# Kernel tuning notes

Measured on AMD Instinct MI355X. Metric: run time of the kernel, lower is better.

Reference implementation:

```python
import jax, jax.numpy as jnp
import numpy as np

B, T, A, F, K, DQ, DV = 64, 1024, 128, 1024, 31, 1024, 512  # filters F == T required by source math


def setup_inputs() -> dict:
    key = jax.random.key(0)
    ks = jax.random.split(key, 8)
    s = 0.05
    return {
        "query": jax.random.normal(ks[0], (B, 1, DQ), jnp.float32),
        "value": jax.random.normal(ks[1], (B, T, DV), jnp.float32),
        "attention_weights_cat": jax.random.uniform(ks[2], (B, T, 2), jnp.float32),
        "Wq": jax.random.normal(ks[3], (DQ, A), jnp.float32) * s,
        "Wm": jax.random.normal(ks[4], (DV, A), jnp.float32) * s,
        "Wv": jax.random.normal(ks[5], (A, 1), jnp.float32) * s,
        "Wconv": jax.random.normal(ks[6], (K, 2, F), jnp.float32) * s,
        "Wloc": jax.random.normal(ks[7], (T, A), jnp.float32) * s,
    }


def reference(query, value, attention_weights_cat, Wq, Wm, Wv, Wconv, Wloc):
    # query_layer: Dense(tanh, no bias): [B,1,DQ] -> [B,1,A]
    q = jnp.tanh(jnp.einsum('bld,da->bla', query, Wq))
    # memory_layer: Dense(tanh, no bias): [B,T,DV] -> [B,T,A]
    v = jnp.tanh(jnp.einsum('btd,da->bta', value, Wm))
    # location conv (SAME, no bias): [B,T,2] -> [B,T,F]
    loc = jax.lax.conv_general_dilated(
        attention_weights_cat, Wconv, window_strides=(1,), padding='SAME',
        dimension_numbers=('NWC', 'WIO', 'NWC'))
    # source transposes [0,2,1] then Dense(T->A, tanh): [B,F,T] -> [B,F,A]
    loc = jnp.tanh(jnp.einsum('bft,ta->bfa', jnp.transpose(loc, (0, 2, 1)), Wloc))
    # additive score (F == T so broadcast add is element-aligned): [B,T,1]
    score = jnp.einsum('bta,ao->bto', jnp.tanh(q + v + loc), Wv)
    alignment = jax.nn.softmax(score, axis=1)                # softmax over time
    context = jnp.sum(alignment * v, axis=1)                  # [B,A]
    return context, jnp.transpose(alignment, (0, 2, 1))       # [B,1,T]
```

## Files before the change

kernel.cpp:

```cpp
#include <hip/hip_runtime.h>
#include <hip/hip_bf16.h>

#define BB 64
#define TT 1024
#define AA 128
#define FF 1024
#define DQ 1024
#define DV 512

typedef __bf16 bf16x8_t __attribute__((ext_vector_type(8)));
typedef __bf16 bf16x4_t __attribute__((ext_vector_type(4)));
typedef float f32x4_t __attribute__((ext_vector_type(4)));
typedef _Float16 f16x4_t __attribute__((ext_vector_type(4)));

__device__ __forceinline__ float ftanh(float x) {
    float e = __expf(2.0f * x);
    return 1.0f - 2.0f / (e + 1.0f);
}

__device__ __forceinline__ __bf16 bhi(float x) { return (__bf16)x; }
__device__ __forceinline__ __bf16 blo(float x) {
    __bf16 h = (__bf16)x;
    return (__bf16)(x - (float)h);
}

__global__ __launch_bounds__(256) void k_prep(
    const float* __restrict__ Wm, const float* __restrict__ Wconv,
    const float* __restrict__ Wloc, const float* __restrict__ query,
    const float* __restrict__ Wq,
    __bf16* __restrict__ pwmhi, __bf16* __restrict__ pwmlo,
    __bf16* __restrict__ wcthi, __bf16* __restrict__ wctlo,
    __bf16* __restrict__ pwlhi, __bf16* __restrict__ pwllo,
    float* __restrict__ q_ws) {
    __shared__ float ls[128 * 65];
    int bx = blockIdx.x, tid = threadIdx.x;
    if (bx < 16) {
        int s = bx, d0 = s * 32;
        for (int i = tid; i < 4096; i += 256) {
            int dd = i >> 7, a = i & 127;
            ls[a * 33 + dd] = Wm[(d0 + dd) * AA + a];
        }
        __syncthreads();
#pragma unroll
        for (int u = 0; u < 2; u++) {
            int pos = tid * 2 + u;
            int l15 = pos & 15, lq = (pos >> 4) & 3, g = pos >> 6;
            bf16x8_t h8, l8;
#pragma unroll
            for (int j = 0; j < 8; j++) {
                float x = ls[(g * 16 + l15) * 33 + lq * 8 + j];
                h8[j] = bhi(x);
                l8[j] = blo(x);
            }
            size_t off = (size_t)(s * 512 + pos) * 8;
            *(bf16x8_t*)(pwmhi + off) = h8;
            *(bf16x8_t*)(pwmlo + off) = l8;
        }
    } else if (bx < 24) {
        int f0 = (bx - 16) * 128;
        for (int i = tid; i < 8192; i += 256) {
            int kc = i >> 7, f = i & 127;
            ls[f * 65 + kc] = (kc < 62) ? Wconv[kc * FF + f0 + f] : 0.f;
        }
        __syncthreads();
        int f = tid >> 1, half = tid & 1;
#pragma unroll
        for (int g = 0; g < 4; g++) {
            bf16x8_t h8, l8;
#pragma unroll
            for (int j = 0; j < 8; j++) {
                float x = ls[f * 65 + half * 32 + g * 8 + j];
                h8[j] = bhi(x);
                l8[j] = blo(x);
            }
            size_t off = (size_t)(f0 + f) * 64 + half * 32 + g * 8;
            *(bf16x8_t*)(wcthi + off) = h8;
            *(bf16x8_t*)(wctlo + off) = l8;
        }
    } else if (bx < 56) {
        int s2 = bx - 24, t0 = s2 * 32;
        for (int i = tid; i < 4096; i += 256) {
            int tt = i >> 7, a = i & 127;
            ls[a * 33 + tt] = Wloc[(t0 + tt) * AA + a];
        }
        __syncthreads();
#pragma unroll
        for (int u = 0; u < 2; u++) {
            int pos = tid * 2 + u;
            int l15 = pos & 15, lq = (pos >> 4) & 3, g = pos >> 6;
            bf16x8_t h8, l8;
#pragma unroll
            for (int j = 0; j < 8; j++) {
                float x = ls[(g * 16 + l15) * 33 + lq * 8 + j];
                h8[j] = bhi(x);
                l8[j] = blo(x);
            }
            size_t off = (size_t)(s2 * 512 + pos) * 8;
            *(bf16x8_t*)(pwlhi + off) = h8;
            *(bf16x8_t*)(pwllo + off) = l8;
        }
    } else {
        int b = bx - 56;
        int a = tid & 127, half = tid >> 7;
        const float* qrow = query + b * DQ + half * 512;
        float a0 = 0.f, a1 = 0.f, a2 = 0.f, a3 = 0.f;
        for (int d = 0; d < 512; d += 4) {
            float4 qv = *(const float4*)(qrow + d);
            int dg = (half * 512 + d) * AA + a;
            a0 += qv.x * Wq[dg];
            a1 += qv.y * Wq[dg + AA];
            a2 += qv.z * Wq[dg + 2 * AA];
            a3 += qv.w * Wq[dg + 3 * AA];
        }
        ls[tid] = a0 + a1 + a2 + a3;
        __syncthreads();
        if (half == 0) q_ws[b * AA + a] = ftanh(ls[a] + ls[a + 128]);
    }
}

__global__ __launch_bounds__(256) void k_zq(
    const float* __restrict__ xcat,
    const __bf16* __restrict__ pwlhi, const __bf16* __restrict__ pwllo,
    float* __restrict__ ztf) {
    int bx = blockIdx.x;
    int b = bx & 63, ahh = (bx >> 6) & 1, kh = bx >> 7;
    int tid = threadIdx.x;
    __shared__ float xs0[1056], xs1[1056];
    __shared__ float zs[64 * 66];
    for (int i = tid; i < 1056; i += 256) {
        int t = i - 16;
        float2 xv = (t >= 0 && t < TT) ? *(const float2*)(xcat + (size_t)(b * TT + t) * 2)
                                       : make_float2(0.f, 0.f);
        xs0[i] = xv.x;
        xs1[i] = xv.y;
    }
    __syncthreads();
    int lane = tid & 63, wid = tid >> 6;
    int wm = wid >> 1, wn = wid & 1;
    int l15 = lane & 15, lq = lane >> 4;

    f32x4_t zacc[2][2];
#pragma unroll
    for (int mi = 0; mi < 2; mi++)
#pragma unroll
        for (int ni = 0; ni < 2; ni++) zacc[mi][ni] = (f32x4_t){0.f, 0.f, 0.f, 0.f};

    int phase = bx & 15;
    for (int sl = 0; sl < 16; sl++) {
        int s = kh * 16 + ((sl + phase) & 15);
        int t0 = s * 32;
        bf16x8_t bh[2], bl[2];
#pragma unroll
        for (int ni = 0; ni < 2; ni++) {
            int g = ahh * 4 + wn * 2 + ni;
            size_t poff = (size_t)((s * 8 + g) * 64 + lane) * 8;
            bh[ni] = *(const bf16x8_t*)(pwlhi + poff);
            bl[ni] = *(const bf16x8_t*)(pwllo + poff);
        }
        bf16x8_t ah_[2], al_[2];
#pragma unroll
        for (int mi = 0; mi < 2; mi++) {
            int kc = wm * 32 + mi * 16 + l15;
            const float* xsc = (kc & 1) ? xs1 : xs0;
            int base = t0 + lq * 8 + (kc >> 1) + 1;
#pragma unroll
            for (int j = 0; j < 8; j++) {
                float x = xsc[base + j];
                ah_[mi][j] = bhi(x);
                al_[mi][j] = blo(x);
            }
        }
#pragma unroll
        for (int ni = 0; ni < 2; ni++)
#pragma unroll
            for (int mi = 0; mi < 2; mi++) {
                zacc[mi][ni] = __builtin_amdgcn_mfma_f32_16x16x32_bf16(ah_[mi], bh[ni], zacc[mi][ni], 0, 0, 0);
                zacc[mi][ni] = __builtin_amdgcn_mfma_f32_16x16x32_bf16(al_[mi], bh[ni], zacc[mi][ni], 0, 0, 0);
                zacc[mi][ni] = __builtin_amdgcn_mfma_f32_16x16x32_bf16(ah_[mi], bl[ni], zacc[mi][ni], 0, 0, 0);
            }
    }
#pragma unroll
    for (int mi = 0; mi < 2; mi++)
#pragma unroll
        for (int ni = 0; ni < 2; ni++)
#pragma unroll
            for (int r = 0; r < 4; r++)
                zs[(wm * 32 + mi * 16 + lq * 4 + r) * 66 + wn * 32 + ni * 16 + l15] = zacc[mi][ni][r];
    __syncthreads();
    int a_local = tid & 63, seg = tid >> 6;
#pragma unroll
    for (int g = 0; g < 2; g++) {
        f32x4_t v0, v1;
#pragma unroll
        for (int j = 0; j < 4; j++) {
            v0[j] = zs[(seg * 16 + g * 8 + j) * 66 + a_local];
            v1[j] = zs[(seg * 16 + g * 8 + 4 + j) * 66 + a_local];
        }
        float* dst = ztf + (size_t)kh * 524288 +
                     ((size_t)b * AA + ahh * 64 + a_local) * 64 + seg * 16 + g * 8;
        *(f32x4_t*)dst = v0;
        *(f32x4_t*)(dst + 4) = v1;
    }
}

__global__ __launch_bounds__(256, 3) void k_main(
    const float* __restrict__ value,
    const __bf16* __restrict__ pwmhi, const __bf16* __restrict__ pwmlo,
    const __bf16* __restrict__ wcthi, const __bf16* __restrict__ wctlo,
    const float* __restrict__ ztf,
    const float* __restrict__ q_ws, const float* __restrict__ Wv,
    _Float16* __restrict__ v_ws, float* __restrict__ score) {
    int b = blockIdx.x >> 3;
    int trow0 = (blockIdx.x & 7) << 7;
    int tid = threadIdx.x;
    int lane = tid & 63, wid = tid >> 6;
    int wm = wid >> 1, wn = wid & 1;
    int l15 = lane & 15, lq = lane >> 4;
    int phase = (blockIdx.x + (blockIdx.x >> 3)) & 15;

    __shared__ __align__(16) float As[2][128 * 32];
    __shared__ float sc_red[256];

    f32x4_t acc[4][4];
#pragma unroll
    for (int mi = 0; mi < 4; mi++)
#pragma unroll
        for (int ni = 0; ni < 4; ni++) acc[mi][ni] = (f32x4_t){0.f, 0.f, 0.f, 0.f};

    int l3 = lane >> 3;
    int su = (lane & 7) ^ l3;
    const float* aG[4];
    unsigned aL[4];
#pragma unroll
    for (int i = 0; i < 4; i++) {
        int row = (wid * 4 + i) * 8 + l3;
        aG[i] = value + (size_t)(b * TT + trow0 + row) * DV + su * 4;
        aL[i] = (unsigned)((wid * 4 + i) * 1024);
    }
    const __bf16* pbh0 = pwmhi + (size_t)(wn * 256 + lane) * 8;
    const __bf16* pbl0 = pwmlo + (size_t)(wn * 256 + lane) * 8;

    bf16x8_t bhb[2][4], blb[2][4];

#define GL4(dst, ptr, OFF) \
    asm volatile("global_load_dwordx4 %0, %1, off offset:" OFF : "=v"(dst) : "v"(ptr))
#define ISSUE_B(bf, s) { \
    const __bf16* _bh = pbh0 + (size_t)(s) * 4096; \
    const __bf16* _bl = pbl0 + (size_t)(s) * 4096; \
    GL4(bhb[bf][0], _bh, "0"); \
    GL4(bhb[bf][1], _bh, "1024"); \
    GL4(bhb[bf][2], _bh, "2048"); \
    GL4(bhb[bf][3], _bh, "3072"); \
    GL4(blb[bf][0], _bl, "0"); \
    GL4(blb[bf][1], _bl, "1024"); \
    GL4(blb[bf][2], _bl, "2048"); \
    GL4(blb[bf][3], _bl, "3072"); }
#define STAGE_A(bf, s)                                                                      \
    {                                                                                       \
        _Pragma("unroll") for (int i = 0; i < 4; i++)                                       \
            __builtin_amdgcn_global_load_lds(                                               \
                (const __attribute__((address_space(1))) void*)(aG[i] + (s) * 32),          \
                (__attribute__((address_space(3))) void*)((char*)&As[bf][0] + aL[i]),       \
                16, 0, 0);                                                                  \
    }

    {
        int s0 = phase & 15;
        ISSUE_B(0, s0);
        STAGE_A(0, s0);
    }

    int swz = l15 & 7;
#pragma unroll
    for (int it = 0; it < 16; ++it) {
        const int cb = it & 1;
        __syncthreads();
        __builtin_amdgcn_sched_barrier(0);

        bf16x8_t ah[4], al[4];
#pragma unroll
        for (int mi = 0; mi < 4; mi++) {
            int row = wm * 64 + mi * 16 + l15;
            const char* rbase = (const char*)&As[cb][0] + row * 128;
            f32x4_t f0 = *(const f32x4_t*)(rbase + (((lq * 2 + 0) ^ swz) << 4));
            f32x4_t f1 = *(const f32x4_t*)(rbase + (((lq * 2 + 1) ^ swz) << 4));
#pragma unroll
            for (int j = 0; j < 4; j++) {
                ah[mi][j] = bhi(f0[j]);
                al[mi][j] = blo(f0[j]);
                ah[mi][4 + j] = bhi(f1[j]);
                al[mi][4 + j] = blo(f1[j]);
            }
        }
        if (it < 15) {
            const int s = (it + 1 + phase) & 15;
            ISSUE_B(cb ^ 1, s);
            STAGE_A(cb ^ 1, s);
        }
#pragma unroll
        for (int mi = 0; mi < 4; mi++)
#pragma unroll
            for (int ni = 0; ni < 4; ni++) {
                acc[mi][ni] = __builtin_amdgcn_mfma_f32_16x16x32_bf16(ah[mi], bhb[cb][ni], acc[mi][ni], 0, 0, 0);
                acc[mi][ni] = __builtin_amdgcn_mfma_f32_16x16x32_bf16(al[mi], bhb[cb][ni], acc[mi][ni], 0, 0, 0);
                acc[mi][ni] = __builtin_amdgcn_mfma_f32_16x16x32_bf16(ah[mi], blb[cb][ni], acc[mi][ni], 0, 0, 0);
            }
    }
#undef ISSUE_B
#undef STAGE_A
#undef GL4

    f32x4_t lacc[4][4];
#pragma unroll
    for (int mi = 0; mi < 4; mi++)
#pragma unroll
        for (int ni = 0; ni < 4; ni++) lacc[mi][ni] = (f32x4_t){0.f, 0.f, 0.f, 0.f};
#pragma unroll
    for (int kc0 = 0; kc0 < 64; kc0 += 32) {
        bf16x8_t a2h[4], a2l[4], b2h[4], b2l[4];
#pragma unroll
        for (int mi = 0; mi < 4; mi++) {
            int f = trow0 + wm * 64 + mi * 16 + l15;
            a2h[mi] = *(const bf16x8_t*)(wcthi + (size_t)f * 64 + kc0 + lq * 8);
            a2l[mi] = *(const bf16x8_t*)(wctlo + (size_t)f * 64 + kc0 + lq * 8);
        }
#pragma unroll
        for (int ni = 0; ni < 4; ni++) {
            int a = wn * 64 + ni * 16 + l15;
            const float* zp = ztf + ((size_t)b * AA + a) * 64 + kc0 + lq * 8;
            f32x4_t z0 = *(const f32x4_t*)zp + *(const f32x4_t*)(zp + 524288);
            f32x4_t z1 = *(const f32x4_t*)(zp + 4) + *(const f32x4_t*)(zp + 524292);
#pragma unroll
            for (int j = 0; j < 4; j++) {
                b2h[ni][j] = bhi(z0[j]);
                b2l[ni][j] = blo(z0[j]);
                b2h[ni][4 + j] = bhi(z1[j]);
                b2l[ni][4 + j] = blo(z1[j]);
            }
        }
#pragma unroll
        for (int mi = 0; mi < 4; mi++)
#pragma unroll
            for (int ni = 0; ni < 4; ni++) {
                lacc[mi][ni] = __builtin_amdgcn_mfma_f32_16x16x32_bf16(a2h[mi], b2h[ni], lacc[mi][ni], 0, 0, 0);
                lacc[mi][ni] = __builtin_amdgcn_mfma_f32_16x16x32_bf16(a2l[mi], b2h[ni], lacc[mi][ni], 0, 0, 0);
                lacc[mi][ni] = __builtin_amdgcn_mfma_f32_16x16x32_bf16(a2h[mi], b2l[ni], lacc[mi][ni], 0, 0, 0);
            }
    }

    float qv[4], wv[4];
#pragma unroll
    for (int ni = 0; ni < 4; ni++) {
        int a = wn * 64 + ni * 16 + l15;
        qv[ni] = q_ws[b * AA + a];
        wv[ni] = Wv[a];
    }
#pragma unroll
    for (int mi = 0; mi < 4; mi++) {
#pragma unroll
        for (int r = 0; r < 4; r++) {
            int tl = wm * 64 + mi * 16 + lq * 4 + r;
            int t = trow0 + tl;
            float s = 0.f;
#pragma unroll
            for (int ni = 0; ni < 4; ni++) {
                float v = ftanh(acc[mi][ni][r]);
                float loc = ftanh(lacc[mi][ni][r]);
                int a = wn * 64 + ni * 16 + l15;
                v_ws[(size_t)(b * TT + t) * AA + a] = (_Float16)v;
                s += ftanh(qv[ni] + v + loc) * wv[ni];
            }
            s += __shfl_xor(s, 1, 64);
            s += __shfl_xor(s, 2, 64);
            s += __shfl_xor(s, 4, 64);
            s += __shfl_xor(s, 8, 64);
            if (l15 == 0) sc_red[wn * 128 + tl] = s;
        }
    }
    __syncthreads();
    if (tid < 128) score[b * TT + trow0 + tid] = sc_red[tid] + sc_red[128 + tid];
}

__global__ void k_softmax(const float* __restrict__ score, float* __restrict__ out_align,
                          float* __restrict__ out_ctx) {
    int b = blockIdx.x, tid = threadIdx.x;
    if (tid < 128) out_ctx[b * AA + tid] = 0.f;
    __shared__ float red[4];
    float s[4];
#pragma unroll
    for (int i = 0; i < 4; i++) s[i] = score[b * TT + tid + i * 256];
    float m = fmaxf(fmaxf(s[0], s[1]), fmaxf(s[2], s[3]));
    for (int off = 32; off; off >>= 1) m = fmaxf(m, __shfl_xor(m, off, 64));
    int wid = tid >> 6;
    if ((tid & 63) == 0) red[wid] = m;
    __syncthreads();
    float M = fmaxf(fmaxf(red[0], red[1]), fmaxf(red[2], red[3]));
    __syncthreads();
    float e[4];
    float sum = 0.f;
#pragma unroll
    for (int i = 0; i < 4; i++) { e[i] = __expf(s[i] - M); sum += e[i]; }
    for (int off = 32; off; off >>= 1) sum += __shfl_xor(sum, off, 64);
    if ((tid & 63) == 0) red[wid] = sum;
    __syncthreads();
    float inv = 1.0f / (red[0] + red[1] + red[2] + red[3]);
#pragma unroll
    for (int i = 0; i < 4; i++) out_align[b * TT + tid + i * 256] = e[i] * inv;
}

__global__ void k_context(const float* __restrict__ align, const _Float16* __restrict__ v_ws,
                          float* __restrict__ out_ctx) {
    int b = blockIdx.y, t0 = blockIdx.x * 64, tid = threadIdx.x;
    int a0 = (tid & 31) * 4, tl = tid >> 5;
    __shared__ float sh[8 * 132];
    f32x4_t acc = (f32x4_t){0.f, 0.f, 0.f, 0.f};
    for (int tt = tl; tt < 64; tt += 8) {
        float w = align[b * TT + t0 + tt];
        f16x4_t vv = *(const f16x4_t*)(v_ws + (size_t)(b * TT + t0 + tt) * AA + a0);
        acc[0] += w * (float)vv[0];
        acc[1] += w * (float)vv[1];
        acc[2] += w * (float)vv[2];
        acc[3] += w * (float)vv[3];
    }
    *(f32x4_t*)&sh[tl * 132 + a0] = acc;
    __syncthreads();
    if (tid < 128) {
        float s = 0.f;
#pragma unroll
        for (int j = 0; j < 8; j++) s += sh[j * 132 + tid];
        atomicAdd(out_ctx + b * AA + tid, s);
    }
}

extern "C" void kernel_launch(void* const* d_in, const int* in_sizes, int n_in,
                              void* d_out, int out_size, void* d_ws, size_t ws_size,
                              hipStream_t stream) {
    const float* query = (const float*)d_in[0];
    const float* value = (const float*)d_in[1];
    const float* xcat  = (const float*)d_in[2];
    const float* Wq    = (const float*)d_in[3];
    const float* Wm    = (const float*)d_in[4];
    const float* Wv    = (const float*)d_in[5];
    const float* Wconv = (const float*)d_in[6];
    const float* Wloc  = (const float*)d_in[7];
    float* out = (float*)d_out;

    float* ws = (float*)d_ws;
    float* q_ws  = ws;
    float* sc_ws = q_ws + 8192;
    _Float16* v_ws = (_Float16*)(sc_ws + 65536);
    __bf16* pwmhi = (__bf16*)(sc_ws + 65536 + 4194304);
    __bf16* pwmlo = pwmhi + 65536;
    __bf16* wcthi = pwmlo + 65536;
    __bf16* wctlo = wcthi + 65536;
    __bf16* pwlhi = wctlo + 65536;
    __bf16* pwllo = pwlhi + 131072;
    float* ztf = (float*)(pwllo + 131072);

    k_prep<<<120, 256, 0, stream>>>(Wm, Wconv, Wloc, query, Wq,
                                    pwmhi, pwmlo, wcthi, wctlo, pwlhi, pwllo, q_ws);
    k_zq<<<256, 256, 0, stream>>>(xcat, pwlhi, pwllo, ztf);
    k_main<<<512, 256, 0, stream>>>(value, pwmhi, pwmlo, wcthi, wctlo, ztf,
                                    q_ws, Wv, v_ws, sc_ws);
    k_softmax<<<BB, 256, 0, stream>>>(sc_ws, out + 8192, out);
    k_context<<<dim3(16, BB), 256, 0, stream>>>(out + 8192, v_ws, out);
}
```

Measured before the change: 279.6 us.

## Halve k_main row tile and stage Wm hi/lo operands through LDS

The main fused GEMM kernel now processes 64 time rows per block instead of 128, doubling the grid to 1024 blocks. The Wm bf16 hi/lo weight fragments are now loaded into shared memory with global_load_lds and double-buffered alongside the value tile, instead of being held in registers per wave. The aim is more parallelism across CUs, lower register pressure, and shared B loads within a block. The cost is a smaller MFMA tile per wave with less reuse, B weights fetched twice as often across the grid, and a full-unroll removal plus a changed barrier placement in the K loop.

```diff
diff --git a/kernel.cpp b/kernel.cpp
--- a/kernel.cpp
+++ b/kernel.cpp
@@ -210,77 +210,68 @@
     const float* __restrict__ ztf,
     const float* __restrict__ q_ws, const float* __restrict__ Wv,
     _Float16* __restrict__ v_ws, float* __restrict__ score) {
-    int b = blockIdx.x >> 3;
-    int trow0 = (blockIdx.x & 7) << 7;
+    int b = blockIdx.x >> 4;
+    int trow0 = (blockIdx.x & 15) << 6;
     int tid = threadIdx.x;
     int lane = tid & 63, wid = tid >> 6;
     int wm = wid >> 1, wn = wid & 1;
     int l15 = lane & 15, lq = lane >> 4;
-    int phase = (blockIdx.x + (blockIdx.x >> 3)) & 15;
-
-    __shared__ __align__(16) float As[2][128 * 32];
-    __shared__ float sc_red[256];
-
-    f32x4_t acc[4][4];
-#pragma unroll
-    for (int mi = 0; mi < 4; mi++)
+    int phase = (blockIdx.x + (blockIdx.x >> 4)) & 15;
+
+    __shared__ __align__(16) float As[2][64 * 32];
+    __shared__ __align__(16) __bf16 Bh[2][512 * 8];
+    __shared__ __align__(16) __bf16 Bl[2][512 * 8];
+    __shared__ float sc_red[128];
+
+    f32x4_t acc[2][4];
+#pragma unroll
+    for (int mi = 0; mi < 2; mi++)
 #pragma unroll
         for (int ni = 0; ni < 4; ni++) acc[mi][ni] = (f32x4_t){0.f, 0.f, 0.f, 0.f};
 
-    int l3 = lane >> 3;
-    int su = (lane & 7) ^ l3;
-    const float* aG[4];
-    unsigned aL[4];
-#pragma unroll
-    for (int i = 0; i < 4; i++) {
-        int row = (wid * 4 + i) * 8 + l3;
+    int su = (tid & 7) ^ ((tid >> 3) & 7);
+    const float* aG[2];
+    unsigned aL[2];
+#pragma unroll
+    for (int i = 0; i < 2; i++) {
+        int row = i * 32 + (tid >> 3);
         aG[i] = value + (size_t)(b * TT + trow0 + row) * DV + su * 4;
-        aL[i] = (unsigned)((wid * 4 + i) * 1024);
-    }
-    const __bf16* pbh0 = pwmhi + (size_t)(wn * 256 + lane) * 8;
-    const __bf16* pbl0 = pwmlo + (size_t)(wn * 256 + lane) * 8;
-
-    bf16x8_t bhb[2][4], blb[2][4];
-
-#define GL4(dst, ptr, OFF) \
-    asm volatile("global_load_dwordx4 %0, %1, off offset:" OFF : "=v"(dst) : "v"(ptr))
-#define ISSUE_B(bf, s) { \
-    const __bf16* _bh = pbh0 + (size_t)(s) * 4096; \
-    const __bf16* _bl = pbl0 + (size_t)(s) * 4096; \
-    GL4(bhb[bf][0], _bh, "0"); \
-    GL4(bhb[bf][1], _bh, "1024"); \
-    GL4(bhb[bf][2], _bh, "2048"); \
-    GL4(bhb[bf][3], _bh, "3072"); \
-    GL4(blb[bf][0], _bl, "0"); \
-    GL4(blb[bf][1], _bl, "1024"); \
-    GL4(blb[bf][2], _bl, "2048"); \
-    GL4(blb[bf][3], _bl, "3072"); }
-#define STAGE_A(bf, s)                                                                      \
-    {                                                                                       \
-        _Pragma("unroll") for (int i = 0; i < 4; i++)                                       \
-            __builtin_amdgcn_global_load_lds(                                               \
-                (const __attribute__((address_space(1))) void*)(aG[i] + (s) * 32),          \
-                (__attribute__((address_space(3))) void*)((char*)&As[bf][0] + aL[i]),       \
-                16, 0, 0);                                                                  \
-    }
-
-    {
-        int s0 = phase & 15;
-        ISSUE_B(0, s0);
-        STAGE_A(0, s0);
-    }
+        aL[i] = (unsigned)((i * 256 + tid) * 16);
+    }
+    unsigned bOffE = (unsigned)tid * 8;
+    unsigned bLB = (unsigned)tid * 16;
+
+#define STAGE(bf, s)                                                                         \
+    {                                                                                        \
+        _Pragma("unroll") for (int i = 0; i < 2; i++)                                        \
+            __builtin_amdgcn_global_load_lds(                                                \
+                (const __attribute__((address_space(1))) void*)(aG[i] + (size_t)(s) * 32),   \
+                (__attribute__((address_space(3))) void*)((char*)&As[bf][0] + aL[i]),        \
+                16, 0, 0);                                                                   \
+        _Pragma("unroll") for (int i = 0; i < 2; i++) {                                      \
+            __builtin_amdgcn_global_load_lds(                                                \
+                (const __attribute__((address_space(1))) void*)(pwmhi + (size_t)(s) * 4096 + bOffE + i * 2048), \
+                (__attribute__((address_space(3))) void*)((char*)&Bh[bf][0] + bLB + i * 4096),                  \
+                16, 0, 0);                                                                   \
+            __builtin_amdgcn_global_load_lds(                                                \
+                (const __attribute__((address_space(1))) void*)(pwmlo + (size_t)(s) * 4096 + bOffE + i * 2048), \
+                (__attribute__((address_space(3))) void*)((char*)&Bl[bf][0] + bLB + i * 4096),                  \
+                16, 0, 0);                                                                   \
+        }                                                                                    \
+    }
+
+    STAGE(0, phase);
+    __syncthreads();
 
     int swz = l15 & 7;
-#pragma unroll
     for (int it = 0; it < 16; ++it) {
-        const int cb = it & 1;
-        __syncthreads();
-        __builtin_amdgcn_sched_barrier(0);
-
-        bf16x8_t ah[4], al[4];
-#pragma unroll
-        for (int mi = 0; mi < 4; mi++) {
-            int row = wm * 64 + mi * 16 + l15;
+        int cb = it & 1;
+        if (it < 15) STAGE(cb ^ 1, (it + 1 + phase) & 15);
+
+        bf16x8_t ah[2], al[2];
+#pragma unroll
+        for (int mi = 0; mi < 2; mi++) {
+            int row = wm * 32 + mi * 16 + l15;
             const char* rbase = (const char*)&As[cb][0] + row * 128;
             f32x4_t f0 = *(const f32x4_t*)(rbase + (((lq * 2 + 0) ^ swz) << 4));
             f32x4_t f1 = *(const f32x4_t*)(rbase + (((lq * 2 + 1) ^ swz) << 4));
@@ -292,35 +283,36 @@
                 al[mi][4 + j] = blo(f1[j]);
             }
         }
-        if (it < 15) {
-            const int s = (it + 1 + phase) & 15;
-            ISSUE_B(cb ^ 1, s);
-            STAGE_A(cb ^ 1, s);
-        }
-#pragma unroll
-        for (int mi = 0; mi < 4; mi++)
+        bf16x8_t bh[4], bl[4];
+#pragma unroll
+        for (int ni = 0; ni < 4; ni++) {
+            int c = (wn * 4 + ni) * 64 + lane;
+            bh[ni] = *(const bf16x8_t*)(&Bh[cb][0] + (size_t)c * 8);
+            bl[ni] = *(const bf16x8_t*)(&Bl[cb][0] + (size_t)c * 8);
+        }
+#pragma unroll
+        for (int mi = 0; mi < 2; mi++)
 #pragma unroll
             for (int ni = 0; ni < 4; ni++) {
-                acc[mi][ni] = __builtin_amdgcn_mfma_f32_16x16x32_bf16(ah[mi], bhb[cb][ni], acc[mi][ni], 0, 0, 0);
-                acc[mi][ni] = __builtin_amdgcn_mfma_f32_16x16x32_bf16(al[mi], bhb[cb][ni], acc[mi][ni], 0, 0, 0);
-                acc[mi][ni] = __builtin_amdgcn_mfma_f32_16x16x32_bf16(ah[mi], blb[cb][ni], acc[mi][ni], 0, 0, 0);
-            }
-    }
-#undef ISSUE_B
-#undef STAGE_A
-#undef GL4
-
-    f32x4_t lacc[4][4];
-#pragma unroll
-    for (int mi = 0; mi < 4; mi++)
+                acc[mi][ni] = __builtin_amdgcn_mfma_f32_16x16x32_bf16(ah[mi], bh[ni], acc[mi][ni], 0, 0, 0);
+                acc[mi][ni] = __builtin_amdgcn_mfma_f32_16x16x32_bf16(al[mi], bh[ni], acc[mi][ni], 0, 0, 0);
+                acc[mi][ni] = __builtin_amdgcn_mfma_f32_16x16x32_bf16(ah[mi], bl[ni], acc[mi][ni], 0, 0, 0);
+            }
+        __syncthreads();
+    }
+#undef STAGE
+
+    f32x4_t lacc[2][4];
+#pragma unroll
+    for (int mi = 0; mi < 2; mi++)
 #pragma unroll
         for (int ni = 0; ni < 4; ni++) lacc[mi][ni] = (f32x4_t){0.f, 0.f, 0.f, 0.f};
 #pragma unroll
     for (int kc0 = 0; kc0 < 64; kc0 += 32) {
-        bf16x8_t a2h[4], a2l[4], b2h[4], b2l[4];
-#pragma unroll
-        for (int mi = 0; mi < 4; mi++) {
-            int f = trow0 + wm * 64 + mi * 16 + l15;
+        bf16x8_t a2h[2], a2l[2], b2h[4], b2l[4];
+#pragma unroll
+        for (int mi = 0; mi < 2; mi++) {
+            int f = trow0 + wm * 32 + mi * 16 + l15;
             a2h[mi] = *(const bf16x8_t*)(wcthi + (size_t)f * 64 + kc0 + lq * 8);
             a2l[mi] = *(const bf16x8_t*)(wctlo + (size_t)f * 64 + kc0 + lq * 8);
         }
@@ -339,7 +331,7 @@
             }
         }
 #pragma unroll
-        for (int mi = 0; mi < 4; mi++)
+        for (int mi = 0; mi < 2; mi++)
 #pragma unroll
             for (int ni = 0; ni < 4; ni++) {
                 lacc[mi][ni] = __builtin_amdgcn_mfma_f32_16x16x32_bf16(a2h[mi], b2h[ni], lacc[mi][ni], 0, 0, 0);
@@ -356,10 +348,10 @@
         wv[ni] = Wv[a];
     }
 #pragma unroll
-    for (int mi = 0; mi < 4; mi++) {
+    for (int mi = 0; mi < 2; mi++) {
 #pragma unroll
         for (int r = 0; r < 4; r++) {
-            int tl = wm * 64 + mi * 16 + lq * 4 + r;
+            int tl = wm * 32 + mi * 16 + lq * 4 + r;
             int t = trow0 + tl;
             float s = 0.f;
 #pragma unroll
@@ -374,11 +366,11 @@
             s += __shfl_xor(s, 2, 64);
             s += __shfl_xor(s, 4, 64);
             s += __shfl_xor(s, 8, 64);
-            if (l15 == 0) sc_red[wn * 128 + tl] = s;
-        }
-    }
-    __syncthreads();
-    if (tid < 128) score[b * TT + trow0 + tid] = sc_red[tid] + sc_red[128 + tid];
+            if (l15 == 0) sc_red[wn * 64 + tl] = s;
+        }
+    }
+    __syncthreads();
+    if (tid < 64) score[b * TT + trow0 + tid] = sc_red[tid] + sc_red[64 + tid];
 }
 
 __global__ void k_softmax(const float* __restrict__ score, float* __restrict__ out_align,
@@ -460,8 +452,8 @@
     k_prep<<<120, 256, 0, stream>>>(Wm, Wconv, Wloc, query, Wq,
                                     pwmhi, pwmlo, wcthi, wctlo, pwlhi, pwllo, q_ws);
     k_zq<<<256, 256, 0, stream>>>(xcat, pwlhi, pwllo, ztf);
-    k_main<<<512, 256, 0, stream>>>(value, pwmhi, pwmlo, wcthi, wctlo, ztf,
-                                    q_ws, Wv, v_ws, sc_ws);
+    k_main<<<1024, 256, 0, stream>>>(value, pwmhi, pwmlo, wcthi, wctlo, ztf,
+                                     q_ws, Wv, v_ws, sc_ws);
     k_softmax<<<BB, 256, 0, stream>>>(sc_ws, out + 8192, out);
     k_context<<<dim3(16, BB), 256, 0, stream>>>(out + 8192, v_ws, out);
 }
```

New measurement: 279.6 us. About the same (-0.0%).
